# Kernel optimization log

Hardware: AMD Instinct MI355X
Metric: run time of the kernel (lower is better)

Reference implementation:

```python
import jax, jax.numpy as jnp
import numpy as np

TEMPERATURE = 0.5

def setup_inputs() -> dict:
    key = jax.random.key(0)
    k1, k2 = jax.random.split(key)
    emb_i = jax.random.normal(k1, (4096, 128), dtype=jnp.float32)
    emb_j = jax.random.normal(k2, (4096, 128), dtype=jnp.float32)
    return {"emb_i": emb_i, "emb_j": emb_j}

def reference(emb_i, emb_j):
    B = emb_i.shape[0]
    eps = 1e-12
    z_i = emb_i / jnp.maximum(jnp.linalg.norm(emb_i, axis=1, keepdims=True), eps)
    z_j = emb_j / jnp.maximum(jnp.linalg.norm(emb_j, axis=1, keepdims=True), eps)
    z = jnp.concatenate([z_i, z_j], axis=0)  # [2B, D]
    # cosine similarity of normalized vectors == dot product (GEMM instead of O(N^2 D) broadcast)
    sim = z @ z.T  # [2B, 2B]
    sim_ij = jnp.einsum('bd,bd->b', z_i, z_j)  # diag(sim, +B)
    positives = jnp.concatenate([sim_ij, sim_ij], axis=0)  # diag(sim,-B) == diag(sim,+B)
    neg_mask = 1.0 - jnp.eye(2 * B, dtype=sim.dtype)
    denom = jnp.sum(neg_mask * jnp.exp(sim / TEMPERATURE), axis=1)  # [2B]
    loss_partial = -(positives / TEMPERATURE - jnp.log(denom))
    return jnp.sum(loss_partial) / (2 * B)
```

## Files before the change

kernel.cpp:

```cpp
#include <hip/hip_runtime.h>
#include <hip/hip_bf16.h>
#include <math.h>

#define BB       4096
#define N2       8192
#define DIMS     128
#define WAVES    4
#define ROWTILES 4
#define ROWS_PER_WAVE   64
#define ROWS_PER_BLOCK  256
#define COL_SPLIT       16
#define COLS_PER_BLOCK  (N2 / COL_SPLIT)
#define CHUNK    64
#define LDS_PAD  8
#define LDS_ROWW (DIMS + LDS_PAD)

#define ZSCALE   1.6986436f
#define DIAG_E2  7.38905609893065f

typedef __attribute__((ext_vector_type(8))) short short8;
typedef __attribute__((ext_vector_type(4))) float float4v;

__global__ __launch_bounds__(256) void norm_kernel(
    const float* __restrict__ emb_i, const float* __restrict__ emb_j,
    __hip_bfloat16* __restrict__ z, float* __restrict__ pos,
    float* __restrict__ denom) {
  if (blockIdx.x < N2 / 256) denom[blockIdx.x * 256 + threadIdx.x] = 0.0f;

  int gw   = (blockIdx.x * blockDim.x + threadIdx.x) >> 6;
  int lane = threadIdx.x & 63;
  if (gw >= BB) return;

  const float2* ei = (const float2*)(emb_i + (size_t)gw * DIMS);
  const float2* ej = (const float2*)(emb_j + (size_t)gw * DIMS);
  float2 a = ei[lane];
  float2 b = ej[lane];

  float sa = a.x * a.x + a.y * a.y;
  float sb = b.x * b.x + b.y * b.y;
  #pragma unroll
  for (int m = 32; m; m >>= 1) {
    sa += __shfl_xor(sa, m, 64);
    sb += __shfl_xor(sb, m, 64);
  }
  float inva = 1.0f / fmaxf(sqrtf(sa), 1e-12f);
  float invb = 1.0f / fmaxf(sqrtf(sb), 1e-12f);

  float zi0 = a.x * inva, zi1 = a.y * inva;
  float zj0 = b.x * invb, zj1 = b.y * invb;

  float p = zi0 * zj0 + zi1 * zj1;
  #pragma unroll
  for (int m = 32; m; m >>= 1) p += __shfl_xor(p, m, 64);
  if (lane == 0) pos[gw] = p;

  __hip_bfloat162* zr_i = (__hip_bfloat162*)(z + (size_t)gw * DIMS);
  __hip_bfloat162* zr_j = (__hip_bfloat162*)(z + (size_t)(gw + BB) * DIMS);
  __hip_bfloat162 vi, vj;
  vi.x = __float2bfloat16(zi0 * ZSCALE); vi.y = __float2bfloat16(zi1 * ZSCALE);
  vj.x = __float2bfloat16(zj0 * ZSCALE); vj.y = __float2bfloat16(zj1 * ZSCALE);
  zr_i[lane] = vi;
  zr_j[lane] = vj;
}

__global__ __launch_bounds__(256, 2) void simloss_main(
    const __hip_bfloat16* __restrict__ z, float* __restrict__ denom) {
  const int blk      = blockIdx.x;
  const int rowBlk   = blk >> 4;
  const int colBlk   = blk & 15;
  const int rowBase  = rowBlk * ROWS_PER_BLOCK;
  const int colBase0 = colBlk * COLS_PER_BLOCK;
  const int tid  = threadIdx.x;
  const int wave = tid >> 6;
  const int lane = tid & 63;
  const int lr   = lane & 15;
  const int quad = lane >> 4;

  __shared__ short lds[CHUNK * LDS_ROWW];

  const ushort* zp = (const ushort*)z;

  short8 afrag[ROWTILES][4];
  #pragma unroll
  for (int rt = 0; rt < ROWTILES; rt++) {
    const int arow = rowBase + wave * ROWS_PER_WAVE + rt * 16 + lr;
    const short8* ap = (const short8*)(zp + (size_t)arow * DIMS + quad * 8);
    afrag[rt][0] = ap[0];
    afrag[rt][1] = ap[4];
    afrag[rt][2] = ap[8];
    afrag[rt][3] = ap[12];
  }

  float rowsum[ROWTILES][4];
  #pragma unroll
  for (int rt = 0; rt < ROWTILES; rt++)
    #pragma unroll
    for (int r = 0; r < 4; r++) rowsum[rt][r] = 0.0f;

  for (int cc = 0; cc < COLS_PER_BLOCK; cc += CHUNK) {
    const int colBase = colBase0 + cc;

    __syncthreads();
    {
      const short8* src = (const short8*)(zp + (size_t)colBase * DIMS);
      #pragma unroll
      for (int i = 0; i < 4; i++) {
        int idx  = tid + 256 * i;
        int row  = idx >> 4;
        int col8 = idx & 15;
        *(short8*)&lds[row * LDS_ROWW + col8 * 8] = src[idx];
      }
    }
    __syncthreads();

    #pragma unroll
    for (int t = 0; t < 4; t++) {
      const short8* bp = (const short8*)&lds[(t * 16 + lr) * LDS_ROWW + quad * 8];
      short8 b0 = bp[0];
      short8 b1 = bp[4];
      short8 b2 = bp[8];
      short8 b3 = bp[12];
      #pragma unroll
      for (int rt = 0; rt < ROWTILES; rt++) {
        float4v acc = {0.0f, 0.0f, 0.0f, 0.0f};
        acc = __builtin_amdgcn_mfma_f32_16x16x32_bf16(afrag[rt][0], b0, acc, 0, 0, 0);
        acc = __builtin_amdgcn_mfma_f32_16x16x32_bf16(afrag[rt][1], b1, acc, 0, 0, 0);
        acc = __builtin_amdgcn_mfma_f32_16x16x32_bf16(afrag[rt][2], b2, acc, 0, 0, 0);
        acc = __builtin_amdgcn_mfma_f32_16x16x32_bf16(afrag[rt][3], b3, acc, 0, 0, 0);
        #pragma unroll
        for (int r = 0; r < 4; r++)
          rowsum[rt][r] += __builtin_amdgcn_exp2f(acc[r]);
      }
    }
  }

  #pragma unroll
  for (int m = 1; m < 16; m <<= 1) {
    #pragma unroll
    for (int rt = 0; rt < ROWTILES; rt++)
      #pragma unroll
      for (int r = 0; r < 4; r++)
        rowsum[rt][r] += __shfl_xor(rowsum[rt][r], m, 64);
  }
  if (lr == 0) {
    #pragma unroll
    for (int rt = 0; rt < ROWTILES; rt++)
      #pragma unroll
      for (int r = 0; r < 4; r++)
        atomicAdd(&denom[rowBase + wave * ROWS_PER_WAVE + rt * 16 + quad * 4 + r],
                  rowsum[rt][r]);
  }
}

__global__ __launch_bounds__(256) void finalize(
    const float* __restrict__ denom, const float* __restrict__ pos,
    float* __restrict__ out) {
  __shared__ double sred[256];
  int tid = threadIdx.x;
  double acc = 0.0;
  for (int r = tid; r < N2; r += 256) {
    acc += (double)(logf(denom[r] - DIAG_E2) - 2.0f * pos[r & (BB - 1)]);
  }
  sred[tid] = acc;
  __syncthreads();
  for (int s = 128; s; s >>= 1) {
    if (tid < s) sred[tid] += sred[tid + s];
    __syncthreads();
  }
  if (tid == 0) out[0] = (float)(sred[0] / (double)N2);
}

extern "C" void kernel_launch(void* const* d_in, const int* in_sizes, int n_in,
                              void* d_out, int out_size, void* d_ws, size_t ws_size,
                              hipStream_t stream) {
  const float* emb_i = (const float*)d_in[0];
  const float* emb_j = (const float*)d_in[1];

  __hip_bfloat16* z = (__hip_bfloat16*)d_ws;
  float* pos   = (float*)((char*)d_ws + (size_t)N2 * DIMS * 2);
  float* denom = (float*)((char*)pos + BB * sizeof(float));

  norm_kernel<<<BB / 4, 256, 0, stream>>>(emb_i, emb_j, z, pos, denom);
  simloss_main<<<(N2 / ROWS_PER_BLOCK) * COL_SPLIT, 256, 0, stream>>>(z, denom);
  finalize<<<1, 256, 0, stream>>>(denom, pos, (float*)d_out);
}
```

Baseline: 91.48 us.

## Exploit symmetry of similarity matrix with triangular tile jobs and fused finalize

Replaces the full 8192x8192 sweep with 128x128 tiles over only the upper triangle, contributing both row and column sums of exp(sim) from each off-diagonal tile, which roughly halves the MFMA and exp work. The separate finalize kernel is folded into the main kernel through a last-block-done counter, removing one launch. In exchange it adds per-tile column reductions through LDS, more atomics on denom, and the triangular index decode.

```diff
diff --git a/kernel.cpp b/kernel.cpp
--- a/kernel.cpp
+++ b/kernel.cpp
@@ -5,13 +5,9 @@
 #define BB       4096
 #define N2       8192
 #define DIMS     128
-#define WAVES    4
-#define ROWTILES 4
-#define ROWS_PER_WAVE   64
-#define ROWS_PER_BLOCK  256
-#define COL_SPLIT       16
-#define COLS_PER_BLOCK  (N2 / COL_SPLIT)
-#define CHUNK    64
+#define NT       64
+#define NJOBS    (NT * (NT + 1) / 2)
+#define TILE     128
 #define LDS_PAD  8
 #define LDS_ROWW (DIMS + LDS_PAD)
 
@@ -24,8 +20,9 @@
 __global__ __launch_bounds__(256) void norm_kernel(
     const float* __restrict__ emb_i, const float* __restrict__ emb_j,
     __hip_bfloat16* __restrict__ z, float* __restrict__ pos,
-    float* __restrict__ denom) {
+    float* __restrict__ denom, unsigned int* __restrict__ cnt) {
   if (blockIdx.x < N2 / 256) denom[blockIdx.x * 256 + threadIdx.x] = 0.0f;
+  if (blockIdx.x == N2 / 256 && threadIdx.x == 0) cnt[0] = 0u;
 
   int gw   = (blockIdx.x * blockDim.x + threadIdx.x) >> 6;
   int lane = threadIdx.x & 63;
@@ -63,27 +60,37 @@
   zr_j[lane] = vj;
 }
 
-__global__ __launch_bounds__(256, 2) void simloss_main(
-    const __hip_bfloat16* __restrict__ z, float* __restrict__ denom) {
-  const int blk      = blockIdx.x;
-  const int rowBlk   = blk >> 4;
-  const int colBlk   = blk & 15;
-  const int rowBase  = rowBlk * ROWS_PER_BLOCK;
-  const int colBase0 = colBlk * COLS_PER_BLOCK;
+__global__ __launch_bounds__(256, 4) void simloss_sym(
+    const __hip_bfloat16* __restrict__ z, float* __restrict__ denom,
+    const float* __restrict__ pos, unsigned int* __restrict__ cnt,
+    float* __restrict__ out) {
+  __shared__ short  lds[TILE * LDS_ROWW];
+  __shared__ float  csum_lds[4][TILE];
+  __shared__ double sred[256];
+  __shared__ int    lastFlag;
+
   const int tid  = threadIdx.x;
   const int wave = tid >> 6;
   const int lane = tid & 63;
   const int lr   = lane & 15;
   const int quad = lane >> 4;
 
-  __shared__ short lds[CHUNK * LDS_ROWW];
+  const int j = blockIdx.x;
+  int I = (int)((129.0f - sqrtf(16641.0f - 8.0f * (float)j)) * 0.5f);
+  I = I < 0 ? 0 : (I > NT - 1 ? NT - 1 : I);
+  while (I < NT - 1 && (I + 1) * (2 * NT - I) / 2 <= j) ++I;
+  while (I > 0 && I * (2 * NT - I + 1) / 2 > j) --I;
+  const int J = I + (j - I * (2 * NT - I + 1) / 2);
+  const bool diag = (I == J);
+  const int R0 = I * TILE;
+  const int C0 = J * TILE;
 
   const ushort* zp = (const ushort*)z;
 
-  short8 afrag[ROWTILES][4];
-  #pragma unroll
-  for (int rt = 0; rt < ROWTILES; rt++) {
-    const int arow = rowBase + wave * ROWS_PER_WAVE + rt * 16 + lr;
+  short8 afrag[2][4];
+  #pragma unroll
+  for (int rt = 0; rt < 2; rt++) {
+    const int arow = R0 + wave * 32 + rt * 16 + lr;
     const short8* ap = (const short8*)(zp + (size_t)arow * DIMS + quad * 8);
     afrag[rt][0] = ap[0];
     afrag[rt][1] = ap[4];
@@ -91,75 +98,90 @@
     afrag[rt][3] = ap[12];
   }
 
-  float rowsum[ROWTILES][4];
-  #pragma unroll
-  for (int rt = 0; rt < ROWTILES; rt++)
+  {
+    const short8* src = (const short8*)(zp + (size_t)C0 * DIMS);
+    #pragma unroll
+    for (int i = 0; i < 8; i++) {
+      int idx  = tid + 256 * i;
+      int row  = idx >> 4;
+      int col8 = idx & 15;
+      *(short8*)&lds[row * LDS_ROWW + col8 * 8] = src[idx];
+    }
+  }
+  __syncthreads();
+
+  float rowsum[2][4];
+  #pragma unroll
+  for (int rt = 0; rt < 2; rt++)
     #pragma unroll
     for (int r = 0; r < 4; r++) rowsum[rt][r] = 0.0f;
 
-  for (int cc = 0; cc < COLS_PER_BLOCK; cc += CHUNK) {
-    const int colBase = colBase0 + cc;
-
-    __syncthreads();
-    {
-      const short8* src = (const short8*)(zp + (size_t)colBase * DIMS);
+  #pragma unroll 2
+  for (int t = 0; t < 8; t++) {
+    const short8* bp = (const short8*)&lds[(t * 16 + lr) * LDS_ROWW + quad * 8];
+    short8 b0 = bp[0];
+    short8 b1 = bp[4];
+    short8 b2 = bp[8];
+    short8 b3 = bp[12];
+    float ctile = 0.0f;
+    #pragma unroll
+    for (int rt = 0; rt < 2; rt++) {
+      float4v acc = {0.0f, 0.0f, 0.0f, 0.0f};
+      acc = __builtin_amdgcn_mfma_f32_16x16x32_bf16(afrag[rt][0], b0, acc, 0, 0, 0);
+      acc = __builtin_amdgcn_mfma_f32_16x16x32_bf16(afrag[rt][1], b1, acc, 0, 0, 0);
+      acc = __builtin_amdgcn_mfma_f32_16x16x32_bf16(afrag[rt][2], b2, acc, 0, 0, 0);
+      acc = __builtin_amdgcn_mfma_f32_16x16x32_bf16(afrag[rt][3], b3, acc, 0, 0, 0);
       #pragma unroll
-      for (int i = 0; i < 4; i++) {
-        int idx  = tid + 256 * i;
-        int row  = idx >> 4;
-        int col8 = idx & 15;
-        *(short8*)&lds[row * LDS_ROWW + col8 * 8] = src[idx];
+      for (int r = 0; r < 4; r++) {
+        float e = __builtin_amdgcn_exp2f(acc[r]);
+        rowsum[rt][r] += e;
+        ctile += e;
       }
     }
-    __syncthreads();
-
-    #pragma unroll
-    for (int t = 0; t < 4; t++) {
-      const short8* bp = (const short8*)&lds[(t * 16 + lr) * LDS_ROWW + quad * 8];
-      short8 b0 = bp[0];
-      short8 b1 = bp[4];
-      short8 b2 = bp[8];
-      short8 b3 = bp[12];
-      #pragma unroll
-      for (int rt = 0; rt < ROWTILES; rt++) {
-        float4v acc = {0.0f, 0.0f, 0.0f, 0.0f};
-        acc = __builtin_amdgcn_mfma_f32_16x16x32_bf16(afrag[rt][0], b0, acc, 0, 0, 0);
-        acc = __builtin_amdgcn_mfma_f32_16x16x32_bf16(afrag[rt][1], b1, acc, 0, 0, 0);
-        acc = __builtin_amdgcn_mfma_f32_16x16x32_bf16(afrag[rt][2], b2, acc, 0, 0, 0);
-        acc = __builtin_amdgcn_mfma_f32_16x16x32_bf16(afrag[rt][3], b3, acc, 0, 0, 0);
-        #pragma unroll
-        for (int r = 0; r < 4; r++)
-          rowsum[rt][r] += __builtin_amdgcn_exp2f(acc[r]);
-      }
-    }
-  }
-
-  #pragma unroll
-  for (int m = 1; m < 16; m <<= 1) {
-    #pragma unroll
-    for (int rt = 0; rt < ROWTILES; rt++)
+    if (!diag) {
+      ctile += __shfl_xor(ctile, 16, 64);
+      ctile += __shfl_xor(ctile, 32, 64);
+      if (quad == 0) csum_lds[wave][t * 16 + lr] = ctile;
+    }
+  }
+
+  #pragma unroll
+  for (int m = 1; m < 16; m <<= 1)
+    #pragma unroll
+    for (int rt = 0; rt < 2; rt++)
       #pragma unroll
       for (int r = 0; r < 4; r++)
         rowsum[rt][r] += __shfl_xor(rowsum[rt][r], m, 64);
-  }
   if (lr == 0) {
     #pragma unroll
-    for (int rt = 0; rt < ROWTILES; rt++)
+    for (int rt = 0; rt < 2; rt++)
       #pragma unroll
       for (int r = 0; r < 4; r++)
-        atomicAdd(&denom[rowBase + wave * ROWS_PER_WAVE + rt * 16 + quad * 4 + r],
-                  rowsum[rt][r]);
-  }
-}
-
-__global__ __launch_bounds__(256) void finalize(
-    const float* __restrict__ denom, const float* __restrict__ pos,
-    float* __restrict__ out) {
-  __shared__ double sred[256];
-  int tid = threadIdx.x;
+        atomicAdd(&denom[R0 + wave * 32 + rt * 16 + quad * 4 + r], rowsum[rt][r]);
+  }
+
+  if (!diag) {
+    __syncthreads();
+    if (tid < TILE) {
+      float s = csum_lds[0][tid] + csum_lds[1][tid] +
+                csum_lds[2][tid] + csum_lds[3][tid];
+      atomicAdd(&denom[C0 + tid], s);
+    }
+  }
+
+  __threadfence();
+  __syncthreads();
+  if (tid == 0) {
+    unsigned int old = atomicAdd(cnt, 1u);
+    lastFlag = (old == (unsigned int)(gridDim.x - 1));
+  }
+  __syncthreads();
+  if (!lastFlag) return;
+
   double acc = 0.0;
   for (int r = tid; r < N2; r += 256) {
-    acc += (double)(logf(denom[r] - DIAG_E2) - 2.0f * pos[r & (BB - 1)]);
+    float d = atomicAdd(&denom[r], 0.0f);
+    acc += (double)(logf(d - DIAG_E2) - 2.0f * pos[r & (BB - 1)]);
   }
   sred[tid] = acc;
   __syncthreads();
@@ -178,9 +200,9 @@
 
   __hip_bfloat16* z = (__hip_bfloat16*)d_ws;
   float* pos   = (float*)((char*)d_ws + (size_t)N2 * DIMS * 2);
-  float* denom = (float*)((char*)pos + BB * sizeof(float));
-
-  norm_kernel<<<BB / 4, 256, 0, stream>>>(emb_i, emb_j, z, pos, denom);
-  simloss_main<<<(N2 / ROWS_PER_BLOCK) * COL_SPLIT, 256, 0, stream>>>(z, denom);
-  finalize<<<1, 256, 0, stream>>>(denom, pos, (float*)d_out);
+  float* denom = pos + BB;
+  unsigned int* cnt = (unsigned int*)(denom + N2);
+
+  norm_kernel<<<BB / 4, 256, 0, stream>>>(emb_i, emb_j, z, pos, denom, cnt);
+  simloss_sym<<<NJOBS, 256, 0, stream>>>(z, denom, pos, cnt, (float*)d_out);
 }
```

After: 206.8 us. 2.26x slower.
